# Optimization experiments

Measured on AMD Instinct MI355X. Metric: run time of the kernel, lower is better.

Reference implementation:

```python
import jax, jax.numpy as jnp
import numpy as np

B, L, E, H, NQ, NC = 64, 201, 512, 512, 10000, 500


def setup_inputs() -> dict:
    key = jax.random.key(0)
    ks = jax.random.split(key, 10)
    s = 0.02
    q = jax.random.randint(ks[0], (B, L), 0, NQ)
    c = jax.random.randint(ks[1], (B, L), 0, NC)
    r = jax.random.randint(ks[2], (B, L), 0, 2)
    qshft = jax.random.randint(ks[3], (B, L - 1), 0, NQ)
    emb = jax.random.normal(ks[4], (2 * NQ, E), dtype=jnp.float32) * s
    W_ih = jax.random.normal(ks[5], (4 * H, E), dtype=jnp.float32) * s
    W_hh = jax.random.normal(ks[6], (4 * H, H), dtype=jnp.float32) * s
    b_ih = jnp.zeros((4 * H,), jnp.float32)
    b_hh = jnp.zeros((4 * H,), jnp.float32)
    W_out = jax.random.normal(ks[7], (NQ, H), dtype=jnp.float32) * s
    b_out = jnp.zeros((NQ,), jnp.float32)
    return {"q": q, "c": c, "r": r, "qshft": qshft, "emb": emb,
            "W_ih": W_ih, "W_hh": W_hh, "b_ih": b_ih, "b_hh": b_hh,
            "W_out": W_out, "b_out": b_out}


def _lstm(xemb, W_ih, W_hh, b_ih, b_hh):
    # xemb: [B, T, E] -> hidden states [B, T, H]. PyTorch gate order: i, f, g, o.
    Bt, T, _ = xemb.shape
    Hd = W_hh.shape[1]
    # precompute input projection for all timesteps (one big GEMM)
    xi = jnp.einsum('bte,ge->btg', xemb, W_ih) + b_ih + b_hh  # [B, T, 4H]

    def step(carry, x_t):
        h, cst = carry
        gates = x_t + h @ W_hh.T  # [B, 4H]
        i, f, g, o = jnp.split(gates, 4, axis=-1)
        i = jax.nn.sigmoid(i)
        f = jax.nn.sigmoid(f)
        g = jnp.tanh(g)
        o = jax.nn.sigmoid(o)
        cst = f * cst + i * g
        h = o * jnp.tanh(cst)
        return (h, cst), h

    h0 = jnp.zeros((Bt, Hd), xemb.dtype)
    _, hs = jax.lax.scan(step, (h0, h0), jnp.swapaxes(xi, 0, 1))
    return jnp.swapaxes(hs, 0, 1)  # [B, T, H]


def reference(q, c, r, qshft, emb, W_ih, W_hh, b_ih, b_hh, W_out, b_out):
    # interaction index: q + num_q * r, dropped last step
    x = (q + NQ * r)[:, :-1]          # [B, T]
    xemb = emb[x]                      # [B, T, E]
    h = _lstm(xemb, W_ih, W_hh, b_ih, b_hh)   # [B, T, H] (dropout = identity in eval)
    y = jax.nn.sigmoid(h @ W_out.T + b_out)   # [B, T, NQ]
    # one-hot(qshft) multiply-sum == gather along last dim
    return jnp.take_along_axis(y, qshft[..., None], axis=-1)[..., 0]  # [B, T]
```

## Files before the change

### kernel.cpp

```cpp
#include <hip/hip_runtime.h>
#include <math.h>

#define B_   64
#define L_   201
#define T_   200
#define E_   512
#define H_   512
#define NQ_  10000
#define G_   2048

#define UGN 32
#define BGN 8
#define LSTM_SMEM (16384 + 65536 + 2048)

__device__ __forceinline__ float sigmoidf_(float x) {
    return 1.0f / (1.0f + __expf(-x));
}

__global__ __launch_bounds__(256) void xi_gemm(const int* __restrict__ q,
                                               const int* __restrict__ r,
                                               const float* __restrict__ emb,
                                               const float* __restrict__ Wih,
                                               const float* __restrict__ bih,
                                               const float* __restrict__ bhh,
                                               float* __restrict__ xi) {
    __shared__ float As[16][68];
    __shared__ float Bs[16][68];
    __shared__ int   rowe[64];

    int tid = threadIdx.x;
    int m0 = blockIdx.x * 64, n0 = blockIdx.y * 64;

    if (tid < 64) {
        int m = m0 + tid;
        int b = m / 200, t = m % 200;
        rowe[tid] = q[b * 201 + t] + NQ_ * r[b * 201 + t];
    }
    __syncthreads();

    int tx = tid & 15, ty = tid >> 4;
    int srow = tid >> 2, skq = tid & 3;

    const float* embA = emb + (size_t)rowe[srow] * 512 + skq * 4;
    const float* WihB = Wih + (size_t)(n0 + srow) * 512 + skq * 4;

    float acc[4][4] = {};

    for (int kt = 0; kt < 32; ++kt) {
        int k0 = kt * 16;
        float4 av = *(const float4*)(embA + k0);
        float4 bv = *(const float4*)(WihB + k0);
        __syncthreads();
        As[skq * 4 + 0][srow] = av.x;
        As[skq * 4 + 1][srow] = av.y;
        As[skq * 4 + 2][srow] = av.z;
        As[skq * 4 + 3][srow] = av.w;
        Bs[skq * 4 + 0][srow] = bv.x;
        Bs[skq * 4 + 1][srow] = bv.y;
        Bs[skq * 4 + 2][srow] = bv.z;
        Bs[skq * 4 + 3][srow] = bv.w;
        __syncthreads();
#pragma unroll
        for (int kk = 0; kk < 16; ++kk) {
            float4 avec = *(const float4*)&As[kk][ty * 4];
            float4 bvec = *(const float4*)&Bs[kk][tx * 4];
            acc[0][0] += avec.x * bvec.x; acc[0][1] += avec.x * bvec.y;
            acc[0][2] += avec.x * bvec.z; acc[0][3] += avec.x * bvec.w;
            acc[1][0] += avec.y * bvec.x; acc[1][1] += avec.y * bvec.y;
            acc[1][2] += avec.y * bvec.z; acc[1][3] += avec.y * bvec.w;
            acc[2][0] += avec.z * bvec.x; acc[2][1] += avec.z * bvec.y;
            acc[2][2] += avec.z * bvec.z; acc[2][3] += avec.z * bvec.w;
            acc[3][0] += avec.w * bvec.x; acc[3][1] += avec.w * bvec.y;
            acc[3][2] += avec.w * bvec.z; acc[3][3] += avec.w * bvec.w;
        }
    }

#pragma unroll
    for (int i = 0; i < 4; ++i) {
        int m = m0 + ty * 4 + i;
        int n = n0 + tx * 4;
        float4 o;
        o.x = acc[i][0] + bih[n + 0] + bhh[n + 0];
        o.y = acc[i][1] + bih[n + 1] + bhh[n + 1];
        o.z = acc[i][2] + bih[n + 2] + bhh[n + 2];
        o.w = acc[i][3] + bih[n + 3] + bhh[n + 3];
        *(float4*)&xi[(size_t)m * G_ + n] = o;
    }
}

__global__ __launch_bounds__(256) void xi_reshape(const float* __restrict__ xi,
                                                  float* __restrict__ xi4) {
    __shared__ float T[64][68];
    int t = blockIdx.x, ug = blockIdx.y;
    int tid = threadIdx.x;
    int b = tid >> 2, gc = tid & 3;
    const float* src = xi + ((size_t)b * 200 + t) * G_ + gc * 512 + ug * 16;
#pragma unroll
    for (int qq = 0; qq < 4; ++qq) {
        float4 v = *(const float4*)(src + qq * 4);
        int row = gc * 16 + qq * 4;
        T[row + 0][b] = v.x; T[row + 1][b] = v.y;
        T[row + 2][b] = v.z; T[row + 3][b] = v.w;
    }
    __syncthreads();
    float* dst = xi4 + ((size_t)t * UGN + ug) * (BGN * 512);
#pragma unroll
    for (int c4 = 0; c4 < 4; ++c4) {
        int d = tid * 16 + c4 * 4;
        int bg = d >> 9, row = (d >> 3) & 63, bl = d & 7;
        float4 v = *(const float4*)&T[row][bg * 8 + bl];
        *(float4*)&dst[d] = v;
    }
}

__global__ __launch_bounds__(256, 1) void lstm3(const float* __restrict__ Whh,
                                                const float* __restrict__ xi4,
                                                float* __restrict__ hb,
                                                float* __restrict__ hsT,
                                                int* __restrict__ bar) {
    extern __shared__ float sm[];
    float* hsl = sm;
    float* P   = sm + 4096;
    float* act = sm + 4096 + 16384;

    const int tid = threadIdx.x;
    const int bid = blockIdx.x;
    const int ug = bid >> 3, bg = bid & 7;
    const int s = tid >> 3, rt = tid & 7;

    float Wreg[8][16];
    {
        const int g = rt >> 1;
#pragma unroll
        for (int i = 0; i < 8; ++i) {
            const int uu = (rt & 1) * 8 + i;
            const float* wr = Whh + (size_t)(g * 512 + ug * 16 + uu) * 512 + s * 16;
            float4 w0 = *(const float4*)(wr + 0);
            float4 w1 = *(const float4*)(wr + 4);
            float4 w2 = *(const float4*)(wr + 8);
            float4 w3 = *(const float4*)(wr + 12);
            Wreg[i][0] = w0.x;  Wreg[i][1] = w0.y;  Wreg[i][2] = w0.z;  Wreg[i][3] = w0.w;
            Wreg[i][4] = w1.x;  Wreg[i][5] = w1.y;  Wreg[i][6] = w1.z;  Wreg[i][7] = w1.w;
            Wreg[i][8] = w2.x;  Wreg[i][9] = w2.y;  Wreg[i][10] = w2.z; Wreg[i][11] = w2.w;
            Wreg[i][12] = w3.x; Wreg[i][13] = w3.y; Wreg[i][14] = w3.z; Wreg[i][15] = w3.w;
        }
    }

    float cst = 0.0f;

    const int o0 = tid * 2;
    const int rrt = o0 >> 6;
    const int cc = (o0 >> 2) & 15;
    const int jj = o0 & 3;
    const int ggate = o0 >> 7;

    for (int t = 0; t < T_; ++t) {
        const float* xig = xi4 + (((size_t)t * UGN + ug) * BGN + bg) * 512;
        const float xv0 = xig[o0];
        const float xv1 = xig[o0 + 1];

        {
            const float* src = hb + ((size_t)(t & 1) * BGN + bg) * 512 * 8 + tid * 16;
            float4 a, b, c, d;
            asm volatile(
                "global_load_dwordx4 %0, %4, off sc0 sc1\n\t"
                "global_load_dwordx4 %1, %4, off offset:16 sc0 sc1\n\t"
                "global_load_dwordx4 %2, %4, off offset:32 sc0 sc1\n\t"
                "global_load_dwordx4 %3, %4, off offset:48 sc0 sc1\n\t"
                "s_waitcnt vmcnt(0)"
                : "=v"(a), "=v"(b), "=v"(c), "=v"(d)
                : "v"(src)
                : "memory");
            const int k0 = tid * 2, k1 = k0 + 1;
            const int kx0 = k0 ^ ((k0 >> 4) & 3);
            const int kx1 = k1 ^ ((k1 >> 4) & 3);
            *(float4*)&hsl[kx0 * 8 + 0] = a;
            *(float4*)&hsl[kx0 * 8 + 4] = b;
            *(float4*)&hsl[kx1 * 8 + 0] = c;
            *(float4*)&hsl[kx1 * 8 + 4] = d;
        }
        __syncthreads();

        float acc[8][8] = {};
        {
            const int sx = s & 3;
#pragma unroll
            for (int kk = 0; kk < 16; ++kk) {
                const int kx = (s * 16 + kk) ^ sx;
                float4 hA = *(float4*)&hsl[kx * 8 + 0];
                float4 hB = *(float4*)&hsl[kx * 8 + 4];
#pragma unroll
                for (int i = 0; i < 8; ++i) {
                    const float w = Wreg[i][kk];
                    acc[i][0] += w * hA.x; acc[i][1] += w * hA.y;
                    acc[i][2] += w * hA.z; acc[i][3] += w * hA.w;
                    acc[i][4] += w * hB.x; acc[i][5] += w * hB.y;
                    acc[i][6] += w * hB.z; acc[i][7] += w * hB.w;
                }
            }
        }

        {
            float* Pr = P + s * 512 + rt * 64;
            const int sw = s & 7;
#pragma unroll
            for (int i = 0; i < 8; ++i) {
                const int c0 = (i * 2) ^ sw;
                const int c1 = (i * 2 + 1) ^ sw;
                *(float4*)&Pr[c0 * 4] = make_float4(acc[i][0], acc[i][1], acc[i][2], acc[i][3]);
                *(float4*)&Pr[c1 * 4] = make_float4(acc[i][4], acc[i][5], acc[i][6], acc[i][7]);
            }
        }
        __syncthreads();

        {
            float s0 = xv0, s1 = xv1;
            const float* Pc = P + rrt * 64 + jj;
#pragma unroll 8
            for (int ss = 0; ss < 32; ++ss) {
                const float* p = Pc + ss * 512 + ((cc ^ (ss & 7)) << 2);
                s0 += p[0];
                s1 += p[1];
            }
            float a0, a1;
            if (ggate == 2) { a0 = tanhf(s0); a1 = tanhf(s1); }
            else            { a0 = sigmoidf_(s0); a1 = sigmoidf_(s1); }
            act[o0] = a0;
            act[o0 + 1] = a1;
        }
        __syncthreads();

        if (tid < 128) {
            const int uu = tid >> 3, bl = tid & 7;
            const float gi = act[(0 * 16 + uu) * 8 + bl];
            const float gf = act[(1 * 16 + uu) * 8 + bl];
            const float gG = act[(2 * 16 + uu) * 8 + bl];
            const float go = act[(3 * 16 + uu) * 8 + bl];
            cst = gf * cst + gi * gG;
            const float h = go * tanhf(cst);
            const int uglob = ug * 16 + uu;
            hsT[((size_t)t * 512 + uglob) * 64 + bg * 8 + bl] = h;
            if (t < T_ - 1) {
                float* dst = hb + (((size_t)((t + 1) & 1) * BGN + bg) * 512 + uglob) * 8 + bl;
                asm volatile("global_store_dword %0, %1, off sc0 sc1"
                             :: "v"(dst), "v"(h) : "memory");
            }
            asm volatile("s_waitcnt vmcnt(0)" ::: "memory");
        }

        if (t < T_ - 1) {
            __syncthreads();
            if (tid == 0) {
                __hip_atomic_fetch_add(&bar[bg * 32], 1, __ATOMIC_RELAXED,
                                       __HIP_MEMORY_SCOPE_AGENT);
                const int target = 32 * (t + 1);
                while (__hip_atomic_load(&bar[bg * 32], __ATOMIC_RELAXED,
                                         __HIP_MEMORY_SCOPE_AGENT) < target)
                    __builtin_amdgcn_s_sleep(2);
            }
            __syncthreads();
        }
    }
}

__global__ __launch_bounds__(256) void out_gather2(const float* __restrict__ hsT,
                                                   const float* __restrict__ Wout,
                                                   const float* __restrict__ bout,
                                                   const int* __restrict__ qshft,
                                                   float* __restrict__ out) {
    __shared__ float red[4][64];
    int t = blockIdx.x;
    int b = threadIdx.x & 63, kg = threadIdx.x >> 6;
    int qs = qshft[b * 200 + t];
    const float* hp = hsT + (size_t)t * 512 * 64 + b;
    const float4* wp = (const float4*)(Wout + (size_t)qs * 512);
    float acc = 0.0f;
    int u0 = kg * 128;
#pragma unroll 8
    for (int u = u0; u < u0 + 128; u += 4) {
        float4 wv = wp[u >> 2];
        acc += hp[(size_t)(u + 0) * 64] * wv.x + hp[(size_t)(u + 1) * 64] * wv.y +
               hp[(size_t)(u + 2) * 64] * wv.z + hp[(size_t)(u + 3) * 64] * wv.w;
    }
    red[kg][b] = acc;
    __syncthreads();
    if (threadIdx.x < 64) {
        int bb = threadIdx.x;
        int qs2 = qshft[bb * 200 + t];
        float sum = red[0][bb] + red[1][bb] + red[2][bb] + red[3][bb];
        out[bb * 200 + t] = sigmoidf_(sum + bout[qs2]);
    }
}

extern "C" void kernel_launch(void* const* d_in, const int* in_sizes, int n_in,
                              void* d_out, int out_size, void* d_ws, size_t ws_size,
                              hipStream_t stream) {
    const int*   q    = (const int*)d_in[0];
    const int*   r    = (const int*)d_in[2];
    const int*   qsft = (const int*)d_in[3];
    const float* emb  = (const float*)d_in[4];
    const float* Wih  = (const float*)d_in[5];
    const float* Whh  = (const float*)d_in[6];
    const float* bih  = (const float*)d_in[7];
    const float* bhh  = (const float*)d_in[8];
    const float* Wout = (const float*)d_in[9];
    const float* bout = (const float*)d_in[10];
    float* out = (float*)d_out;

    char* wsb = (char*)d_ws;
    int*   bar = (int*)wsb;
    float* hb  = (float*)(wsb + 1024);
    float* hsT = (float*)(wsb + 1024 + 262144);
    float* xi4 = (float*)(wsb + 1024 + 262144 + 26214400ull);
    float* xi  = (float*)(wsb + 1024 + 262144 + 26214400ull + 104857600ull);

    hipMemsetAsync(wsb, 0, 1024 + 262144, stream);

    xi_gemm<<<dim3(200, 32), 256, 0, stream>>>(q, r, emb, Wih, bih, bhh, xi);
    xi_reshape<<<dim3(200, 32), 256, 0, stream>>>(xi, xi4);

    hipFuncSetAttribute((const void*)lstm3,
                        hipFuncAttributeMaxDynamicSharedMemorySize, LSTM_SMEM);
    {
        const float* a0 = Whh; const float* a1 = xi4; float* a2 = hb;
        float* a3 = hsT; int* a4 = bar;
        void* ka[] = {(void*)&a0, (void*)&a1, (void*)&a2, (void*)&a3, (void*)&a4};
        hipError_t e = hipLaunchCooperativeKernel((const void*)lstm3, dim3(256),
                                                  dim3(256), ka, LSTM_SMEM, stream);
        if (e != hipSuccess) {
            lstm3<<<256, 256, LSTM_SMEM, stream>>>(Whh, xi4, hb, hsT, bar);
        }
    }

    out_gather2<<<200, 256, 0, stream>>>(hsT, Wout, bout, qsft, out);
}
```

Before: 2.650 ms.

## Replace atomic-counter grid barrier with per-block flags and simplify gate reduction layout

Each block now publishes its step number to its own padded flag, and 32 threads poll the flags of the blocks in the same batch group. This replaces the single contended atomic counter per group that one thread spun on. The gate-sum reduction now maps one thread to a fixed gate column, removing the per-gate branch, and the h exchange buffer uses a contiguous per-unit-group layout. hsT now shares workspace with the xi buffer, which is no longer needed once the LSTM runs, so the workspace shrinks. The risk is extra polling traffic from 32 lanes per block.

```diff
diff --git a/kernel.cpp b/kernel.cpp
--- a/kernel.cpp
+++ b/kernel.cpp
@@ -113,7 +113,7 @@
     }
 }
 
-__global__ __launch_bounds__(256, 1) void lstm3(const float* __restrict__ Whh,
+__global__ __launch_bounds__(256, 1) void lstm4(const float* __restrict__ Whh,
                                                 const float* __restrict__ xi4,
                                                 float* __restrict__ hb,
                                                 float* __restrict__ hsT,
@@ -147,20 +147,17 @@
     }
 
     float cst = 0.0f;
-
-    const int o0 = tid * 2;
-    const int rrt = o0 >> 6;
-    const int cc = (o0 >> 2) & 15;
-    const int jj = o0 & 3;
-    const int ggate = o0 >> 7;
+    const bool isTanh = (tid < 128);
+
+    int* myflag = bar + (bg * 32 + ug) * 8;
 
     for (int t = 0; t < T_; ++t) {
         const float* xig = xi4 + (((size_t)t * UGN + ug) * BGN + bg) * 512;
-        const float xv0 = xig[o0];
-        const float xv1 = xig[o0 + 1];
+        const float xv1 = xig[tid];
+        const float xv2 = xig[tid + 256];
 
         {
-            const float* src = hb + ((size_t)(t & 1) * BGN + bg) * 512 * 8 + tid * 16;
+            const float* src = hb + ((size_t)(t & 1) * BGN + bg) * 4096 + tid * 16;
             float4 a, b, c, d;
             asm volatile(
                 "global_load_dwordx4 %0, %4, off sc0 sc1\n\t"
@@ -214,34 +211,32 @@
         __syncthreads();
 
         {
-            float s0 = xv0, s1 = xv1;
-            const float* Pc = P + rrt * 64 + jj;
+            float s1v = xv1, s2v = xv2;
 #pragma unroll 8
             for (int ss = 0; ss < 32; ++ss) {
-                const float* p = Pc + ss * 512 + ((cc ^ (ss & 7)) << 2);
-                s0 += p[0];
-                s1 += p[1];
-            }
-            float a0, a1;
-            if (ggate == 2) { a0 = tanhf(s0); a1 = tanhf(s1); }
-            else            { a0 = sigmoidf_(s0); a1 = sigmoidf_(s1); }
-            act[o0] = a0;
-            act[o0 + 1] = a1;
+                const int swz = (ss & 7) << 2;
+                const float* Prow = P + ss * 512;
+                s1v += Prow[tid ^ swz];
+                s2v += Prow[(tid + 256) ^ swz];
+            }
+            const float a1 = sigmoidf_(s1v);
+            const float a2 = isTanh ? tanhf(s2v) : sigmoidf_(s2v);
+            act[tid] = a1;
+            act[tid + 256] = a2;
         }
         __syncthreads();
 
         if (tid < 128) {
-            const int uu = tid >> 3, bl = tid & 7;
-            const float gi = act[(0 * 16 + uu) * 8 + bl];
-            const float gf = act[(1 * 16 + uu) * 8 + bl];
-            const float gG = act[(2 * 16 + uu) * 8 + bl];
-            const float go = act[(3 * 16 + uu) * 8 + bl];
-            cst = gf * cst + gi * gG;
+            const float gi = act[tid];
+            const float gf = act[tid + 128];
+            const float gg = act[tid + 256];
+            const float go = act[tid + 384];
+            cst = gf * cst + gi * gg;
             const float h = go * tanhf(cst);
-            const int uglob = ug * 16 + uu;
-            hsT[((size_t)t * 512 + uglob) * 64 + bg * 8 + bl] = h;
+            const int uglob = ug * 16 + (tid >> 3);
+            hsT[((size_t)t * 512 + uglob) * 64 + bg * 8 + (tid & 7)] = h;
             if (t < T_ - 1) {
-                float* dst = hb + (((size_t)((t + 1) & 1) * BGN + bg) * 512 + uglob) * 8 + bl;
+                float* dst = hb + ((size_t)((t + 1) & 1) * BGN + bg) * 4096 + ug * 128 + tid;
                 asm volatile("global_store_dword %0, %1, off sc0 sc1"
                              :: "v"(dst), "v"(h) : "memory");
             }
@@ -250,13 +245,13 @@
 
         if (t < T_ - 1) {
             __syncthreads();
-            if (tid == 0) {
-                __hip_atomic_fetch_add(&bar[bg * 32], 1, __ATOMIC_RELAXED,
-                                       __HIP_MEMORY_SCOPE_AGENT);
-                const int target = 32 * (t + 1);
-                while (__hip_atomic_load(&bar[bg * 32], __ATOMIC_RELAXED,
-                                         __HIP_MEMORY_SCOPE_AGENT) < target)
-                    __builtin_amdgcn_s_sleep(2);
+            if (tid == 0)
+                __hip_atomic_store(myflag, t + 1, __ATOMIC_RELAXED,
+                                   __HIP_MEMORY_SCOPE_AGENT);
+            if (tid < 32) {
+                while (__hip_atomic_load(bar + (bg * 32 + tid) * 8, __ATOMIC_RELAXED,
+                                         __HIP_MEMORY_SCOPE_AGENT) < t + 1)
+                    __builtin_amdgcn_s_sleep(1);
             }
             __syncthreads();
         }
@@ -309,26 +304,27 @@
 
     char* wsb = (char*)d_ws;
     int*   bar = (int*)wsb;
-    float* hb  = (float*)(wsb + 1024);
-    float* hsT = (float*)(wsb + 1024 + 262144);
-    float* xi4 = (float*)(wsb + 1024 + 262144 + 26214400ull);
-    float* xi  = (float*)(wsb + 1024 + 262144 + 26214400ull + 104857600ull);
-
-    hipMemsetAsync(wsb, 0, 1024 + 262144, stream);
+    float* hb  = (float*)(wsb + 8192);
+    float* xi4 = (float*)(wsb + 8192 + 262144);
+    float* xiX = (float*)(wsb + 8192 + 262144 + 104857600ull);
+    float* xi  = xiX;
+    float* hsT = xiX;
+
+    hipMemsetAsync(wsb, 0, 8192 + 262144, stream);
 
     xi_gemm<<<dim3(200, 32), 256, 0, stream>>>(q, r, emb, Wih, bih, bhh, xi);
     xi_reshape<<<dim3(200, 32), 256, 0, stream>>>(xi, xi4);
 
-    hipFuncSetAttribute((const void*)lstm3,
+    hipFuncSetAttribute((const void*)lstm4,
                         hipFuncAttributeMaxDynamicSharedMemorySize, LSTM_SMEM);
     {
         const float* a0 = Whh; const float* a1 = xi4; float* a2 = hb;
         float* a3 = hsT; int* a4 = bar;
         void* ka[] = {(void*)&a0, (void*)&a1, (void*)&a2, (void*)&a3, (void*)&a4};
-        hipError_t e = hipLaunchCooperativeKernel((const void*)lstm3, dim3(256),
+        hipError_t e = hipLaunchCooperativeKernel((const void*)lstm4, dim3(256),
                                                   dim3(256), ka, LSTM_SMEM, stream);
         if (e != hipSuccess) {
-            lstm3<<<256, 256, LSTM_SMEM, stream>>>(Whh, xi4, hb, hsT, bar);
+            lstm4<<<256, 256, LSTM_SMEM, stream>>>(Whh, xi4, hb, hsT, bar);
         }
     }
 
```

After: 2.611 ms. No clear change (-1.4%).
